# Optimization experiments

Measured on AMD Instinct MI355X. Metric: run time of the kernel, lower is better.

Reference implementation:

```python
import jax, jax.numpy as jnp
import numpy as np

B, D, H = 131072, 128, 64  # batch, input_dim (down_ch), output_dim


def _lstm(x, h, c, w_ih, w_hh, b):
    # torch nn.LSTMCell math; gate order i, f, g, o
    gates = x @ w_ih.T + h @ w_hh.T + b
    i, f, g, o = jnp.split(gates, 4, axis=-1)
    c2 = jax.nn.sigmoid(f) * c + jax.nn.sigmoid(i) * jnp.tanh(g)
    h2 = jax.nn.sigmoid(o) * jnp.tanh(c2)
    return h2, c2


def _lstm0(x, w_ih, b):
    # LSTMCell with zero initial (h, c): h-term and f*c term vanish
    gates = x @ w_ih.T + b
    i, f, g, o = jnp.split(gates, 4, axis=-1)
    c2 = jax.nn.sigmoid(i) * jnp.tanh(g)
    h2 = jax.nn.sigmoid(o) * jnp.tanh(c2)
    return h2, c2


def _trans(x, w, stride):
    # trans(): Conv1d(1,1,k=3,stride,pad=1,bias=False) + softmax(dim=-1)
    # x: [N, W], w: [1, 1, 3]
    y = jax.lax.conv_general_dilated(x[:, None, :], w, (stride,), [(1, 1)],
                                     dimension_numbers=('NCH', 'OIH', 'NCH'))
    return jax.nn.softmax(y[:, 0, :], axis=-1)


def _forward(spec, fw_ih1, fw_hh1, fb1, fw_ih2, fw_hh2, fb2, fw_ih3, fw_hh3, fb3,
             fw_ih4, fw_hh4, fb4, bw_ih1, bw_hh1, bb1, bw_ih2, bw_hh2, bb2,
             bw_ih3, bw_hh3, bb3, bw_ih4, bw_hh4, bb4,
             ft12h, ft12c, ft23h, ft23c, ft34h,
             bt43h, bt43c, bt32h, bt32c, bt21h, bt21c):
    b = spec.shape[0]
    # multi-scale chunking of spec: x2=[b,2,64], x3=[b,4,32], x4=[b,8,16]
    x2 = spec.reshape(b, 2, D // 2)
    x3 = spec.reshape(b, 4, D // 4)
    x4 = spec.reshape(b, 8, D // 8)

    # ---- fwd_LSTM (short memory): coarse -> fine, trans stride 2 ----
    # every cell call uses a state taken from the previous scale's backup, so
    # all steps at a scale are independent -> fully vectorized over steps.
    h1, c1 = _lstm0(spec, fw_ih1, fb1)                                      # [b,64]
    hb = _trans(h1, ft12h, 2)                                               # [b,32]
    cb = _trans(c1, ft12c, 2)
    h2, c2 = _lstm(x2, hb[:, None, :], cb[:, None, :], fw_ih2, fw_hh2, fb2)  # [b,2,32]
    hb2 = _trans(h2.reshape(b * 2, 32), ft23h, 2).reshape(b, 2, 16)
    cb2 = _trans(c2.reshape(b * 2, 32), ft23c, 2).reshape(b, 2, 16)
    h3, c3 = _lstm(x3, jnp.repeat(hb2, 2, axis=1), jnp.repeat(cb2, 2, axis=1),
                   fw_ih3, fw_hh3, fb3)                                     # [b,4,16]
    hb3 = _trans(h3.reshape(b * 4, 16), ft34h, 2).reshape(b, 4, 8)
    cb3 = _trans(c3.reshape(b * 4, 16), ft34h, 2).reshape(b, 4, 8)  # original bug: trans3_4h reused for cx
    h4, _ = _lstm(x4, jnp.repeat(hb3, 2, axis=1), jnp.repeat(cb3, 2, axis=1),
                  fw_ih4, fw_hh4, fb4)                                      # [b,8,8]
    out_fwd = h4.reshape(b, 64)

    # ---- bwd_LSTM (long memory): fine -> coarse, trans stride 1 over pairs ----
    h4b, c4b = _lstm0(x4, bw_ih4, bb4)                                      # [b,8,8] (zero state each step)
    # pairs of consecutive steps concatenated along features == reshape(b,4,16)
    hb4 = _trans(h4b.reshape(b * 4, 16), bt43h, 1).reshape(b, 4, 16)
    cb4 = _trans(c4b.reshape(b * 4, 16), bt43c, 1).reshape(b, 4, 16)
    h3b, c3b = _lstm(x3, hb4, cb4, bw_ih3, bw_hh3, bb3)                     # [b,4,16]
    hb3b = _trans(h3b.reshape(b * 2, 32), bt32h, 1).reshape(b, 2, 32)
    cb3b = _trans(c3b.reshape(b * 2, 32), bt32c, 1).reshape(b, 2, 32)
    h2b, c2b = _lstm(x2, hb3b, cb3b, bw_ih2, bw_hh2, bb2)                   # [b,2,32]
    hb1b = _trans(h2b.reshape(b, 64), bt21h, 1)                             # [b,64]
    cb1b = _trans(c2b.reshape(b, 64), bt21c, 1)
    _, c1b = _lstm(spec, hb1b, cb1b, bw_ih1, bw_hh1, bb1)                   # [b,64]

    return jnp.concatenate([out_fwd, c1b], axis=-1)                         # [b,128]


def setup_inputs() -> dict:
    key = jax.random.key(0)
    ks = iter(jax.random.split(key, 64))

    def nrm(shape, s=0.08):
        return (jax.random.normal(next(ks), shape) * s).astype(jnp.float32)

    inp = {"spec": jax.random.normal(next(ks), (B, D), dtype=jnp.float32)}
    dims = [(D, H), (D // 2, H // 2), (D // 4, H // 4), (D // 8, H // 8)]
    for pre in ("f", "b"):
        for idx, (di, dh) in enumerate(dims, 1):
            inp[f"{pre}w_ih{idx}"] = nrm((4 * dh, di))
            inp[f"{pre}w_hh{idx}"] = nrm((4 * dh, dh))
            inp[f"{pre}b{idx}"] = nrm((4 * dh,))
    for name in ("ft12h", "ft12c", "ft23h", "ft23c", "ft34h",
                 "bt43h", "bt43c", "bt32h", "bt32c", "bt21h", "bt21c"):
        inp[name] = nrm((1, 1, 3), 0.5)
    return inp


def reference(spec, fw_ih1, fw_hh1, fb1, fw_ih2, fw_hh2, fb2, fw_ih3, fw_hh3, fb3,
              fw_ih4, fw_hh4, fb4, bw_ih1, bw_hh1, bb1, bw_ih2, bw_hh2, bb2,
              bw_ih3, bw_hh3, bb3, bw_ih4, bw_hh4, bb4,
              ft12h, ft12c, ft23h, ft23c, ft34h,
              bt43h, bt43c, bt32h, bt32c, bt21h, bt21c):
    return _forward(spec, fw_ih1, fw_hh1, fb1, fw_ih2, fw_hh2, fb2, fw_ih3, fw_hh3,
                    fb3, fw_ih4, fw_hh4, fb4, bw_ih1, bw_hh1, bb1, bw_ih2, bw_hh2,
                    bb2, bw_ih3, bw_hh3, bb3, bw_ih4, bw_hh4, bb4,
                    ft12h, ft12c, ft23h, ft23c, ft34h,
                    bt43h, bt43c, bt32h, bt32c, bt21h, bt21c)
```

## Files before the change

### kernel.cpp

```cpp
#include <hip/hip_runtime.h>

typedef __attribute__((ext_vector_type(4))) float f32x4;
typedef __attribute__((ext_vector_type(8))) short short8;

#define DEV __device__ __forceinline__

DEV float fastrcp(float x){ return __builtin_amdgcn_rcpf(x); }
DEV float sigm(float x){ return fastrcp(1.f + __expf(-x)); }
DEV float tanh_(float x){ return 1.f - 2.f*fastrcp(__expf(2.f*x)+1.f); }
DEV unsigned short f2bf(float f){ unsigned u=__float_as_uint(f); u += 0x7fffu + ((u>>16)&1u); return (unsigned short)(u>>16); }
DEV float bf2f(unsigned short h){ return __uint_as_float(((unsigned)h)<<16); }
DEV unsigned pack2(float a, float b){ return (unsigned)f2bf(a) | ((unsigned)f2bf(b)<<16); }

DEV int gmask(int f){ return ((f&1)<<5) | (f&2) | ((f&4)<<2); }
DEV void stBF(char* A, int f, int b, float v){ *(unsigned short*)(A + (((f<<6) + (b ^ gmask(f)))<<1)) = f2bf(v); }
DEV float ldBF(const char* A, int f, int b){ return bf2f(*(const unsigned short*)(A + (((f<<6) + (b ^ gmask(f)))<<1))); }

DEV short8 frag(const char* p){ return *(const short8*)p; }
DEV short8 gfrag(const char* p){ return *(const short8*)p; }
DEV f32x4 MF(short8 a, short8 b, f32x4 c){ return __builtin_amdgcn_mfma_f32_16x16x32_bf16(a,b,c,0,0,0); }

struct P {
  const float *spec;
  const float *fw_ih1,*fw_hh1,*fb1,*fw_ih2,*fw_hh2,*fb2,*fw_ih3,*fw_hh3,*fb3,*fw_ih4,*fw_hh4,*fb4;
  const float *bw_ih1,*bw_hh1,*bb1,*bw_ih2,*bw_hh2,*bb2,*bw_ih3,*bw_hh3,*bb3,*bw_ih4,*bw_hh4,*bb4;
  const float *ft12h,*ft12c,*ft23h,*ft23c,*ft34h,*bt43h,*bt43c,*bt32h,*bt32c,*bt21h,*bt21c;
  float *out;
};

#define OF1 0
#define OF2 48
#define OF3 72
#define OF4 80
#define OB4 86
#define OB3 90
#define OB2 98
#define OB1 122
#define BLOBB (194*1024)

__global__ __launch_bounds__(256) void dsgsf_prep(P p, char* blob){
  int s = blockIdx.x;
  if (s == 3 || s == 4){
    bool isF = (s == 3);
    const float* wih = isF ? p.fw_ih4 : p.bw_ih4;
    const float* whh = p.fw_hh4;
    int nslot = isF ? 6 : 4;
    int off   = isF ? OF4 : OB4;
    for (int n = threadIdx.x; n < nslot*64; n += 256){
      int st = n>>6, lx = n&63;
      int R = lx&15, half = R>>3, feat = R&7;
      int k0 = ((lx>>4)<<3);
      unsigned dw[4];
      #pragma unroll
      for (int q=0;q<4;++q){
        float a=0.f, bv=0.f;
        int ka=k0+2*q, kb=ka+1;
        if (isF){
          if (st < 4){
            int pp = st>>1, t = st&1;
            int gi = t*2 + half;
            int src = gi*8 + feat, base = pp*16;
            if (ka>=base && ka<base+16) a  = wih[src*16 + (ka-base)];
            if (kb>=base && kb<base+16) bv = wih[src*16 + (kb-base)];
          } else {
            int t = st-4; int gi = t*2 + half; int src = gi*8 + feat;
            if (ka<8) a  = whh[src*8+ka];
            if (kb<8) bv = whh[src*8+kb];
          }
        } else {
          int pp = st>>1, t = st&1;
          int gi = (t==0) ? (half? 2:0) : (half? -1:3);
          if (gi >= 0){
            int src = gi*8 + feat, base = pp*16;
            if (ka>=base && ka<base+16) a  = wih[src*16 + (ka-base)];
            if (kb>=base && kb<base+16) bv = wih[src*16 + (kb-base)];
          }
        }
        dw[q] = pack2(a,bv);
      }
      *(uint4*)(blob + (size_t)(off+st)*1024 + lx*16) = make_uint4(dw[0],dw[1],dw[2],dw[3]);
    }
    return;
  }
  const float* wih=nullptr; const float* whh=nullptr;
  int H=0,NG=0,Kx=0,KXT=0,Kh=0,KT=0,NT=0,off=0,o0=0,o1=1,o2=2,o3=3;
  switch(s){
    case 0: wih=p.fw_ih1;               H=64;NG=3;Kx=128;KXT=4;Kh=0; KT=4;NT=12;off=OF1;o1=2;o2=3; break;
    case 1: wih=p.fw_ih2; whh=p.fw_hh2; H=32;NG=4;Kx=64; KXT=2;Kh=32;KT=3;NT=8; off=OF2; break;
    case 2: wih=p.fw_ih3; whh=p.fw_hh3; H=16;NG=4;Kx=32; KXT=1;Kh=16;KT=2;NT=4; off=OF3; break;
    case 5: wih=p.bw_ih3; whh=p.bw_hh3; H=16;NG=4;Kx=32; KXT=1;Kh=16;KT=2;NT=4; off=OB3; break;
    case 6: wih=p.bw_ih2; whh=p.bw_hh2; H=32;NG=4;Kx=64; KXT=2;Kh=32;KT=3;NT=8; off=OB2; break;
    default:wih=p.bw_ih1; whh=p.bw_hh1; H=64;NG=3;Kx=128;KXT=4;Kh=64;KT=6;NT=12;off=OB1; break;
  }
  int total = KT*NT*64;
  for (int n = threadIdx.x; n < total; n += 256){
    int kt = n/(NT*64); int rem = n - kt*NT*64; int nt = rem>>6; int lx = rem&63;
    int R = nt*16 + (lx&15);
    int gi = R / H; int feat = R - gi*H;
    int og = (gi==0)? o0 : (gi==1)? o1 : (gi==2)? o2 : o3;
    int src = og*H + feat;
    int k0 = kt*32 + ((lx>>4)<<3);
    unsigned dw[4];
    #pragma unroll
    for (int q=0;q<4;++q){
      float a=0.f, b=0.f;
      int ka=k0+2*q, kb=ka+1;
      if (gi < NG){
        if (ka < Kx) a = wih[(size_t)src*Kx + ka];
        else { int kh = ka - KXT*32; if (kh>=0 && kh<Kh) a = whh[(size_t)src*Kh + kh]; }
        if (kb < Kx) b = wih[(size_t)src*Kx + kb];
        else { int kh = kb - KXT*32; if (kh>=0 && kh<Kh) b = whh[(size_t)src*Kh + kh]; }
      }
      dw[q] = pack2(a,b);
    }
    *(uint4*)(blob + (size_t)off*1024 + (size_t)(kt*NT + nt)*1024 + lx*16) =
        make_uint4(dw[0],dw[1],dw[2],dw[3]);
  }
}

template<int NG,int NFT,int KT, class AF>
DEV void gemm_reg(f32x4 (&acc)[2][NG], const char* bstage, int nf, int mtp, int l, AF af){
  constexpr int NT = NG*NFT;
  #pragma unroll
  for (int kt=0; kt<KT; ++kt){
    short8 a0 = af(kt, mtp*2);
    short8 a1 = af(kt, mtp*2+1);
    #pragma unroll
    for (int g=0; g<NG; ++g){
      short8 bf = gfrag(bstage + (size_t)(kt*NT + g*NFT + nf)*1024 + l*16);
      acc[0][g] = MF(a0, bf, acc[0][g]);
      acc[1][g] = MF(a1, bf, acc[1][g]);
    }
  }
}

template<int NG>
DEV void binit(f32x4 (&acc)[2][NG], const float* bias, int H, int feat,
               int o0, int o1, int o2, int o3){
  int og[4] = {o0,o1,o2,o3};
  #pragma unroll
  for (int g=0; g<NG; ++g){
    float bv = bias[og[g]*H + feat];
    f32x4 v = {bv,bv,bv,bv};
    acc[0][g]=v; acc[1][g]=v;
  }
}

DEV void pw4(const f32x4 (&acc)[2][4], char* AH, char* AC, const char* BC,
             int arow, int cbrow, int mtp, int l){
  #pragma unroll
  for (int mtI=0;mtI<2;++mtI){
    #pragma unroll
    for (int r=0;r<4;++r){
      int batch = (mtp*2+mtI)*16 + ((l>>4)<<2) + r;
      float cb = ldBF(BC, cbrow, batch);
      float c = sigm(acc[mtI][1][r])*cb + sigm(acc[mtI][0][r])*tanh_(acc[mtI][2][r]);
      float h = sigm(acc[mtI][3][r])*tanh_(c);
      stBF(AH, arow, batch, h);
      stBF(AC, arow, batch, c);
    }
  }
}

template<int L,int S,int NO>
DEV void convE(const char* Ain, int row0, const float* tw, int o0, int b,
               float (&y)[NO], float& s){
  float w0=tw[0], w1=tw[1], w2=tw[2];
  s = 0.f;
  #pragma unroll
  for (int j=0;j<NO;++j){
    int o=o0+j, c=S*o;
    float v = w1*ldBF(Ain,row0+c,b);
    if (c>=1)   v += w0*ldBF(Ain,row0+c-1,b);
    if (c+1<L)  v += w2*ldBF(Ain,row0+c+1,b);
    y[j] = __expf(v); s += y[j];
  }
}
template<int SZ,int NO>
DEV void wrTF(char* TFb, int subBase, int o0, int b, const float (&y)[NO], float inv){
  #pragma unroll
  for (int g8=0; g8<NO/8; ++g8){
    int oo = o0 + g8*8, fl = oo&31;
    char* base = TFb + (size_t)((subBase+(oo>>5))*4+(b>>4))*SZ + ((b&15)+16*(fl>>3))*16;
    unsigned d0=pack2(y[g8*8+0]*inv,y[g8*8+1]*inv), d1=pack2(y[g8*8+2]*inv,y[g8*8+3]*inv);
    unsigned d2=pack2(y[g8*8+4]*inv,y[g8*8+5]*inv), d3=pack2(y[g8*8+6]*inv,y[g8*8+7]*inv);
    *(uint4*)base = make_uint4(d0,d1,d2,d3);
  }
}
template<int NO>
DEV void wrBC(char* BCb, int row0, int b, const float (&y)[NO], float inv){
  #pragma unroll
  for (int j=0;j<NO;++j) stBF(BCb, row0+j, b, y[j]*inv);
}

__global__ __launch_bounds__(512, 4) void dsgsf_main(P p, const char* blob){
  __shared__ __align__(16) char SM[51200];
  char* XP = SM;
  char* AH = SM + 16384;
  char* AC = SM + 24576;
  char* BC = SM + 32768;
  char* TF = SM + 40960;
  float* PSm = (float*)(SM + 49152);

  const int tid = threadIdx.x;
  const int l   = tid & 63;
  const int wu  = __builtin_amdgcn_readfirstlane(tid >> 6);
  const int mtp = wu & 1, z = wu >> 1;
  const long b0 = (long)blockIdx.x * 64;

  #pragma unroll
  for (int it=0; it<2; ++it){
    int n = it*512 + tid; int slot = n>>6, lx = n&63;
    int kc = slot>>2, mt = slot&3;
    const float* sp = p.spec + (b0 + mt*16 + (lx&15))*128 + kc*32 + ((lx>>4)<<3);
    float4 v0 = *(const float4*)sp; float4 v1 = *(const float4*)(sp+4);
    unsigned* dst = (unsigned*)(XP + (size_t)slot*1024 + lx*16);
    dst[0]=pack2(v0.x,v0.y); dst[1]=pack2(v0.z,v0.w);
    dst[2]=pack2(v1.x,v1.y); dst[3]=pack2(v1.z,v1.w);
  }
  __syncthreads();

  {
    f32x4 acc[2][3];
    int feat = z*16 + (l&15);
    binit<3>(acc, p.fb1, 64, feat, 0,2,3,0);
    auto af = [&](int kt, int mt){ return frag(XP + (size_t)((kt<<2)+mt)*1024 + l*16); };
    gemm_reg<3,4,4>(acc, blob + (size_t)OF1*1024, z, mtp, l, af);
    #pragma unroll
    for (int mtI=0;mtI<2;++mtI)
      #pragma unroll
      for (int r=0;r<4;++r){
        int batch = (mtp*2+mtI)*16 + ((l>>4)<<2) + r;
        float c = sigm(acc[mtI][0][r])*tanh_(acc[mtI][1][r]);
        float h = sigm(acc[mtI][2][r])*tanh_(c);
        stBF(AH, feat, batch, h); stBF(AC, feat, batch, c);
      }
  }
  __syncthreads();

  {
    float y[8], s;
    if (wu<4) convE<64,2,8>(AH, 0, p.ft12h, wu*8, l, y, s);
    else      convE<64,2,8>(AC, 0, p.ft12c, (wu-4)*8, l, y, s);
    PSm[wu*64+l] = s;
    __syncthreads();
    float tot = (wu<4) ? PSm[0*64+l]+PSm[1*64+l]+PSm[2*64+l]+PSm[3*64+l]
                       : PSm[4*64+l]+PSm[5*64+l]+PSm[6*64+l]+PSm[7*64+l];
    float inv = fastrcp(tot);
    if (wu<4) wrTF<1024,8>(TF, 0, wu*8, l, y, inv);
    else      wrBC<8>(BC, (wu-4)*8, l, y, inv);
  }
  __syncthreads();

  {
    f32x4 acc[2][4];
    int step = z>>1, nf = z&1;
    int feat = nf*16 + (l&15);
    binit<4>(acc, p.fb2, 32, feat, 0,1,2,3);
    auto af = [&](int kt, int mt){
      return (kt<2) ? frag(XP + (size_t)(((2*step+kt)<<2)+mt)*1024 + l*16)
                    : frag(TF + (size_t)mt*1024 + l*16); };
    gemm_reg<4,2,3>(acc, blob + (size_t)OF2*1024, nf, mtp, l, af);
    pw4(acc, AH, AC, BC, step*32+feat, feat, mtp, l);
  }
  __syncthreads();

  {
    float y[8], s; int v=wu&3, st=v>>1, ch=v&1;
    if (wu<4) convE<32,2,8>(AH, st*32, p.ft23h, ch*8, l, y, s);
    else      convE<32,2,8>(AC, st*32, p.ft23c, ch*8, l, y, s);
    PSm[wu*64+l] = s;
    __syncthreads();
    int base = (wu&4) | (st<<1);
    float inv = fastrcp(PSm[base*64+l] + PSm[(base|1)*64+l]);
    if (wu<4) wrTF<512,8>(TF, st, ch*8, l, y, inv);
    else      wrBC<8>(BC, st*16+ch*8, l, y, inv);
  }
  __syncthreads();

  {
    f32x4 acc[2][4];
    int s = z, feat = l&15;
    binit<4>(acc, p.fb3, 16, feat, 0,1,2,3);
    auto af = [&](int kt, int mt){
      return (kt==0) ? frag(XP + (size_t)((s<<2)+mt)*1024 + l*16)
                     : frag(TF + (size_t)(((s>>1)<<2)+mt)*512 + (l&31)*16); };
    gemm_reg<4,1,2>(acc, blob + (size_t)OF3*1024, 0, mtp, l, af);
    pw4(acc, AH, AC, BC, s*16+feat, (s>>1)*16+feat, mtp, l);
  }
  __syncthreads();

  {
    float y[8], s;
    if (wu<4){ convE<16,2,8>(AH, wu*16, p.ft34h, 0, l, y, s);
               wrTF<256,8>(TF, wu, 0, l, y, fastrcp(s)); }
    else     { convE<16,2,8>(AC, (wu-4)*16, p.ft34h, 0, l, y, s);
               wrBC<8>(BC, (wu-4)*8, l, y, fastrcp(s)); }
  }
  __syncthreads();

  {
    f32x4 a4[2][2][2];
    float bv0 = p.fb4[l&15], bv1 = p.fb4[16+(l&15)];
    #pragma unroll
    for (int uu=0;uu<2;++uu)
      #pragma unroll
      for (int mtI=0;mtI<2;++mtI){ a4[uu][mtI][0]=f32x4{bv0,bv0,bv0,bv0}; a4[uu][mtI][1]=f32x4{bv1,bv1,bv1,bv1}; }
    const char* bs = blob + (size_t)OF4*1024;
    short8 A0 = frag(XP + (size_t)((z<<2)+mtp*2  )*1024 + l*16);
    short8 A1 = frag(XP + (size_t)((z<<2)+mtp*2+1)*1024 + l*16);
    short8 H0 = frag(TF + (size_t)((z<<2)+mtp*2  )*256 + (l&15)*16);
    short8 H1 = frag(TF + (size_t)((z<<2)+mtp*2+1)*256 + (l&15)*16);
    short8 bh0 = gfrag(bs + 4*1024 + l*16);
    short8 bh1 = gfrag(bs + 5*1024 + l*16);
    #pragma unroll
    for (int uu=0;uu<2;++uu){
      short8 bx0 = gfrag(bs + (uu*2+0)*1024 + l*16);
      short8 bx1 = gfrag(bs + (uu*2+1)*1024 + l*16);
      a4[uu][0][0]=MF(A0,bx0,a4[uu][0][0]); a4[uu][0][1]=MF(A0,bx1,a4[uu][0][1]);
      a4[uu][1][0]=MF(A1,bx0,a4[uu][1][0]); a4[uu][1][1]=MF(A1,bx1,a4[uu][1][1]);
      a4[uu][0][0]=MF(H0,bh0,a4[uu][0][0]); a4[uu][0][1]=MF(H0,bh1,a4[uu][0][1]);
      a4[uu][1][0]=MF(H1,bh0,a4[uu][1][0]); a4[uu][1][1]=MF(H1,bh1,a4[uu][1][1]);
    }
    #pragma unroll
    for (int uu=0;uu<2;++uu)
      #pragma unroll
      for (int mtI=0;mtI<2;++mtI)
        #pragma unroll
        for (int r=0;r<4;++r){
          float iv = a4[uu][mtI][0][r], gv = a4[uu][mtI][1][r];
          float xf = __shfl_xor(iv,8), xo = __shfl_xor(gv,8);
          if ((l&15)<8){
            int q = l&15, u = z*2+uu;
            int batch = (mtp*2+mtI)*16 + ((l>>4)<<2) + r;
            float cb = ldBF(BC, (u>>1)*8+q, batch);
            float c = sigm(xf)*cb + sigm(iv)*tanh_(gv);
            float h = sigm(xo)*tanh_(c);
            p.out[(size_t)(b0+batch)*128 + u*8 + q] = h;
          }
        }
  }

  {
    f32x4 a4[2][2][2];
    float bv0 = ((l&15)<8) ? p.bb4[l&15] : p.bb4[(l&15)+8];
    float bv1 = ((l&15)<8) ? p.bb4[24+(l&15)] : 0.f;
    #pragma unroll
    for (int uu=0;uu<2;++uu)
      #pragma unroll
      for (int mtI=0;mtI<2;++mtI){ a4[uu][mtI][0]=f32x4{bv0,bv0,bv0,bv0}; a4[uu][mtI][1]=f32x4{bv1,bv1,bv1,bv1}; }
    const char* bs = blob + (size_t)OB4*1024;
    short8 A0 = frag(XP + (size_t)((z<<2)+mtp*2  )*1024 + l*16);
    short8 A1 = frag(XP + (size_t)((z<<2)+mtp*2+1)*1024 + l*16);
    #pragma unroll
    for (int uu=0;uu<2;++uu){
      short8 bx0 = gfrag(bs + (uu*2+0)*1024 + l*16);
      short8 bx1 = gfrag(bs + (uu*2+1)*1024 + l*16);
      a4[uu][0][0]=MF(A0,bx0,a4[uu][0][0]); a4[uu][0][1]=MF(A0,bx1,a4[uu][0][1]);
      a4[uu][1][0]=MF(A1,bx0,a4[uu][1][0]); a4[uu][1][1]=MF(A1,bx1,a4[uu][1][1]);
    }
    #pragma unroll
    for (int uu=0;uu<2;++uu)
      #pragma unroll
      for (int mtI=0;mtI<2;++mtI)
        #pragma unroll
        for (int r=0;r<4;++r){
          float iv = a4[uu][mtI][0][r], ov = a4[uu][mtI][1][r];
          float gv = __shfl_xor(iv,8);
          if ((l&15)<8){
            int q = l&15, u = z*2+uu;
            int batch = (mtp*2+mtI)*16 + ((l>>4)<<2) + r;
            float c = sigm(iv)*tanh_(gv);
            float h = sigm(ov)*tanh_(c);
            stBF(AH, u*8+q, batch, h); stBF(AC, u*8+q, batch, c);
          }
        }
  }
  __syncthreads();

  {
    float y[16], s;
    if (wu<4){ convE<16,1,16>(AH, wu*16, p.bt43h, 0, l, y, s);
               wrTF<512,16>(TF, wu, 0, l, y, fastrcp(s)); }
    else     { convE<16,1,16>(AC, (wu-4)*16, p.bt43c, 0, l, y, s);
               wrBC<16>(BC, (wu-4)*16, l, y, fastrcp(s)); }
  }
  __syncthreads();

  {
    f32x4 acc[2][4];
    int s = z, feat = l&15;
    binit<4>(acc, p.bb3, 16, feat, 0,1,2,3);
    auto af = [&](int kt, int mt){
      return (kt==0) ? frag(XP + (size_t)((s<<2)+mt)*1024 + l*16)
                     : frag(TF + (size_t)((s<<2)+mt)*512 + (l&31)*16); };
    gemm_reg<4,1,2>(acc, blob + (size_t)OB3*1024, 0, mtp, l, af);
    pw4(acc, AH, AC, BC, s*16+feat, s*16+feat, mtp, l);
  }
  __syncthreads();

  {
    float y[16], s; int v=wu&3, st=v>>1, ch=v&1;
    if (wu<4) convE<32,1,16>(AH, st*32, p.bt32h, ch*16, l, y, s);
    else      convE<32,1,16>(AC, st*32, p.bt32c, ch*16, l, y, s);
    PSm[wu*64+l] = s;
    __syncthreads();
    int base = (wu&4) | (st<<1);
    float inv = fastrcp(PSm[base*64+l] + PSm[(base|1)*64+l]);
    if (wu<4) wrTF<1024,16>(TF, st, ch*16, l, y, inv);
    else      wrBC<16>(BC, st*32+ch*16, l, y, inv);
  }
  __syncthreads();

  {
    f32x4 acc[2][4];
    int t2 = z>>1, nf = z&1;
    int feat = nf*16 + (l&15);
    binit<4>(acc, p.bb2, 32, feat, 0,1,2,3);
    auto af = [&](int kt, int mt){
      return (kt<2) ? frag(XP + (size_t)(((2*t2+kt)<<2)+mt)*1024 + l*16)
                    : frag(TF + (size_t)((t2<<2)+mt)*1024 + l*16); };
    gemm_reg<4,2,3>(acc, blob + (size_t)OB2*1024, nf, mtp, l, af);
    pw4(acc, AH, AC, BC, t2*32+feat, t2*32+feat, mtp, l);
  }
  __syncthreads();

  {
    float y[16], s;
    if (wu<4) convE<64,1,16>(AH, 0, p.bt21h, wu*16, l, y, s);
    else      convE<64,1,16>(AC, 0, p.bt21c, (wu-4)*16, l, y, s);
    PSm[wu*64+l] = s;
    __syncthreads();
    float tot = (wu<4) ? PSm[0*64+l]+PSm[1*64+l]+PSm[2*64+l]+PSm[3*64+l]
                       : PSm[4*64+l]+PSm[5*64+l]+PSm[6*64+l]+PSm[7*64+l];
    float inv = fastrcp(tot);
    if (wu<4) wrTF<1024,16>(TF, 0, wu*16, l, y, inv);
    else      wrBC<16>(BC, (wu-4)*16, l, y, inv);
  }
  __syncthreads();

  {
    f32x4 acc[2][3];
    int feat = z*16 + (l&15);
    binit<3>(acc, p.bb1, 64, feat, 0,1,2,0);
    auto af = [&](int kt, int mt){
      return (kt<4) ? frag(XP + (size_t)((kt<<2)+mt)*1024 + l*16)
                    : frag(TF + (size_t)(((kt-4)<<2)+mt)*1024 + l*16); };
    gemm_reg<3,4,6>(acc, blob + (size_t)OB1*1024, z, mtp, l, af);
    #pragma unroll
    for (int mtI=0;mtI<2;++mtI)
      #pragma unroll
      for (int r=0;r<4;++r){
        int batch = (mtp*2+mtI)*16 + ((l>>4)<<2) + r;
        float cb = ldBF(BC, feat, batch);
        float c = sigm(acc[mtI][1][r])*cb + sigm(acc[mtI][0][r])*tanh_(acc[mtI][2][r]);
        p.out[(size_t)(b0+batch)*128 + 64 + feat] = c;
      }
  }
}

extern "C" void kernel_launch(void* const* d_in, const int* in_sizes, int n_in,
                              void* d_out, int out_size, void* d_ws, size_t ws_size,
                              hipStream_t stream) {
  if (ws_size < (size_t)BLOBB) return;
  P p;
  p.spec   = (const float*)d_in[0];
  p.fw_ih1 = (const float*)d_in[1];  p.fw_hh1 = (const float*)d_in[2];  p.fb1 = (const float*)d_in[3];
  p.fw_ih2 = (const float*)d_in[4];  p.fw_hh2 = (const float*)d_in[5];  p.fb2 = (const float*)d_in[6];
  p.fw_ih3 = (const float*)d_in[7];  p.fw_hh3 = (const float*)d_in[8];  p.fb3 = (const float*)d_in[9];
  p.fw_ih4 = (const float*)d_in[10]; p.fw_hh4 = (const float*)d_in[11]; p.fb4 = (const float*)d_in[12];
  p.bw_ih1 = (const float*)d_in[13]; p.bw_hh1 = (const float*)d_in[14]; p.bb1 = (const float*)d_in[15];
  p.bw_ih2 = (const float*)d_in[16]; p.bw_hh2 = (const float*)d_in[17]; p.bb2 = (const float*)d_in[18];
  p.bw_ih3 = (const float*)d_in[19]; p.bw_hh3 = (const float*)d_in[20]; p.bb3 = (const float*)d_in[21];
  p.bw_ih4 = (const float*)d_in[22]; p.bw_hh4 = (const float*)d_in[23]; p.bb4 = (const float*)d_in[24];
  p.ft12h = (const float*)d_in[25]; p.ft12c = (const float*)d_in[26];
  p.ft23h = (const float*)d_in[27]; p.ft23c = (const float*)d_in[28];
  p.ft34h = (const float*)d_in[29];
  p.bt43h = (const float*)d_in[30]; p.bt43c = (const float*)d_in[31];
  p.bt32h = (const float*)d_in[32]; p.bt32c = (const float*)d_in[33];
  p.bt21h = (const float*)d_in[34]; p.bt21c = (const float*)d_in[35];
  p.out = (float*)d_out;

  char* blob = (char*)d_ws;
  hipLaunchKernelGGL(dsgsf_prep, dim3(8), dim3(256), 0, stream, p, blob);
  int Bn = in_sizes[0] / 128;
  hipLaunchKernelGGL(dsgsf_main, dim3(Bn/64), dim3(512), 0, stream, p, (const char*)blob);
}
```

Measured before the change: 179.1 us.

## Use hardware bf16 pack, exp2 intrinsics, paired LDS stores and sliding-window convs

Replaces the manual round-to-nearest bf16 conversion with the v_cvt_pk_bf16_f32 instruction and switches sigmoid/tanh/softmax exponentials to the raw exp2 intrinsic with folded log2e scaling. Pointwise LSTM epilogues now pack two batch elements per 32-bit LDS store instead of 16-bit stores. The conv+softmax helpers are split into stride-1 and stride-2 versions that reuse loaded neighbours in a sliding window, removing redundant LDS loads and boundary branches. Together these cut ALU and LDS instruction count in an elementwise-heavy fused kernel, at the cost of relying on paired stores landing contiguously under the swizzle and slightly different rounding of the exp path.

```diff
diff --git a/kernel.cpp b/kernel.cpp
--- a/kernel.cpp
+++ b/kernel.cpp
@@ -6,14 +6,20 @@
 #define DEV __device__ __forceinline__
 
 DEV float fastrcp(float x){ return __builtin_amdgcn_rcpf(x); }
-DEV float sigm(float x){ return fastrcp(1.f + __expf(-x)); }
-DEV float tanh_(float x){ return 1.f - 2.f*fastrcp(__expf(2.f*x)+1.f); }
-DEV unsigned short f2bf(float f){ unsigned u=__float_as_uint(f); u += 0x7fffu + ((u>>16)&1u); return (unsigned short)(u>>16); }
+DEV float exp2r(float x){ return __builtin_amdgcn_exp2f(x); }
+DEV float sigm(float x){ return fastrcp(1.f + exp2r(x*-1.44269504f)); }
+DEV float tanh_(float x){ return 1.f - 2.f*fastrcp(exp2r(x*2.88539008f)+1.f); }
+
+DEV unsigned cvtpk(float lo, float hi){ unsigned r; asm("v_cvt_pk_bf16_f32 %0, %1, %2" : "=v"(r) : "v"(lo), "v"(hi)); return r; }
+DEV unsigned short f2bf(float f){ return (unsigned short)cvtpk(f,f); }
 DEV float bf2f(unsigned short h){ return __uint_as_float(((unsigned)h)<<16); }
-DEV unsigned pack2(float a, float b){ return (unsigned)f2bf(a) | ((unsigned)f2bf(b)<<16); }
+DEV unsigned pack2(float a, float b){ return cvtpk(a,b); }
 
 DEV int gmask(int f){ return ((f&1)<<5) | (f&2) | ((f&4)<<2); }
 DEV void stBF(char* A, int f, int b, float v){ *(unsigned short*)(A + (((f<<6) + (b ^ gmask(f)))<<1)) = f2bf(v); }
+DEV void stBFpair(char* A, int f, int b, float v0, float v1){
+  *(unsigned*)(A + (((f<<6) + (b ^ gmask(f)))<<1)) = cvtpk(v0, v1);
+}
 DEV float ldBF(const char* A, int f, int b){ return bf2f(*(const unsigned short*)(A + (((f<<6) + (b ^ gmask(f)))<<1))); }
 
 DEV short8 frag(const char* p){ return *(const short8*)p; }
@@ -150,30 +156,53 @@
              int arow, int cbrow, int mtp, int l){
   #pragma unroll
   for (int mtI=0;mtI<2;++mtI){
+    float hv[4], cv[4];
+    int bb = (mtp*2+mtI)*16 + ((l>>4)<<2);
     #pragma unroll
     for (int r=0;r<4;++r){
-      int batch = (mtp*2+mtI)*16 + ((l>>4)<<2) + r;
-      float cb = ldBF(BC, cbrow, batch);
-      float c = sigm(acc[mtI][1][r])*cb + sigm(acc[mtI][0][r])*tanh_(acc[mtI][2][r]);
-      float h = sigm(acc[mtI][3][r])*tanh_(c);
-      stBF(AH, arow, batch, h);
-      stBF(AC, arow, batch, c);
-    }
-  }
-}
-
-template<int L,int S,int NO>
-DEV void convE(const char* Ain, int row0, const float* tw, int o0, int b,
-               float (&y)[NO], float& s){
-  float w0=tw[0], w1=tw[1], w2=tw[2];
+      float cb = ldBF(BC, cbrow, bb + r);
+      cv[r] = sigm(acc[mtI][1][r])*cb + sigm(acc[mtI][0][r])*tanh_(acc[mtI][2][r]);
+      hv[r] = sigm(acc[mtI][3][r])*tanh_(cv[r]);
+    }
+    stBFpair(AH, arow, bb,   hv[0], hv[1]);
+    stBFpair(AH, arow, bb+2, hv[2], hv[3]);
+    stBFpair(AC, arow, bb,   cv[0], cv[1]);
+    stBFpair(AC, arow, bb+2, cv[2], cv[3]);
+  }
+}
+
+template<int L,int NO>
+DEV void convE1(const char* Ain, int row0, const float* tw, int o0, int b,
+                float (&y)[NO], float& s){
+  float w0=tw[0]*1.44269504f, w1=tw[1]*1.44269504f, w2=tw[2]*1.44269504f;
   s = 0.f;
+  float prev = (o0 >= 1) ? ldBF(Ain, row0+o0-1, b) : 0.f;
+  float cur  = ldBF(Ain, row0+o0, b);
   #pragma unroll
   for (int j=0;j<NO;++j){
-    int o=o0+j, c=S*o;
-    float v = w1*ldBF(Ain,row0+c,b);
-    if (c>=1)   v += w0*ldBF(Ain,row0+c-1,b);
-    if (c+1<L)  v += w2*ldBF(Ain,row0+c+1,b);
-    y[j] = __expf(v); s += y[j];
+    int c = o0 + j;
+    float nxt;
+    if (j < NO-1) nxt = ldBF(Ain, row0+c+1, b);
+    else          nxt = (o0+NO < L) ? ldBF(Ain, row0+c+1, b) : 0.f;
+    float v = w0*prev + w1*cur + w2*nxt;
+    y[j] = exp2r(v); s += y[j];
+    prev = cur; cur = nxt;
+  }
+}
+template<int L,int NO>
+DEV void convE2(const char* Ain, int row0, const float* tw, int o0, int b,
+                float (&y)[NO], float& s){
+  float w0=tw[0]*1.44269504f, w1=tw[1]*1.44269504f, w2=tw[2]*1.44269504f;
+  s = 0.f;
+  float left = (o0 >= 1) ? ldBF(Ain, row0+2*o0-1, b) : 0.f;
+  #pragma unroll
+  for (int j=0;j<NO;++j){
+    int c = 2*(o0+j);
+    float mid = ldBF(Ain, row0+c,   b);
+    float rgt = ldBF(Ain, row0+c+1, b);
+    float v = w0*left + w1*mid + w2*rgt;
+    y[j] = exp2r(v); s += y[j];
+    left = rgt;
   }
 }
 template<int SZ,int NO>
@@ -182,8 +211,8 @@
   for (int g8=0; g8<NO/8; ++g8){
     int oo = o0 + g8*8, fl = oo&31;
     char* base = TFb + (size_t)((subBase+(oo>>5))*4+(b>>4))*SZ + ((b&15)+16*(fl>>3))*16;
-    unsigned d0=pack2(y[g8*8+0]*inv,y[g8*8+1]*inv), d1=pack2(y[g8*8+2]*inv,y[g8*8+3]*inv);
-    unsigned d2=pack2(y[g8*8+4]*inv,y[g8*8+5]*inv), d3=pack2(y[g8*8+6]*inv,y[g8*8+7]*inv);
+    unsigned d0=cvtpk(y[g8*8+0]*inv,y[g8*8+1]*inv), d1=cvtpk(y[g8*8+2]*inv,y[g8*8+3]*inv);
+    unsigned d2=cvtpk(y[g8*8+4]*inv,y[g8*8+5]*inv), d3=cvtpk(y[g8*8+6]*inv,y[g8*8+7]*inv);
     *(uint4*)base = make_uint4(d0,d1,d2,d3);
   }
 }
@@ -214,9 +243,9 @@
     int kc = slot>>2, mt = slot&3;
     const float* sp = p.spec + (b0 + mt*16 + (lx&15))*128 + kc*32 + ((lx>>4)<<3);
     float4 v0 = *(const float4*)sp; float4 v1 = *(const float4*)(sp+4);
-    unsigned* dst = (unsigned*)(XP + (size_t)slot*1024 + lx*16);
-    dst[0]=pack2(v0.x,v0.y); dst[1]=pack2(v0.z,v0.w);
-    dst[2]=pack2(v1.x,v1.y); dst[3]=pack2(v1.z,v1.w);
+    unsigned d0=cvtpk(v0.x,v0.y), d1=cvtpk(v0.z,v0.w);
+    unsigned d2=cvtpk(v1.x,v1.y), d3=cvtpk(v1.z,v1.w);
+    *(uint4*)(XP + (size_t)slot*1024 + lx*16) = make_uint4(d0,d1,d2,d3);
   }
   __syncthreads();
 
@@ -227,21 +256,26 @@
     auto af = [&](int kt, int mt){ return frag(XP + (size_t)((kt<<2)+mt)*1024 + l*16); };
     gemm_reg<3,4,4>(acc, blob + (size_t)OF1*1024, z, mtp, l, af);
     #pragma unroll
-    for (int mtI=0;mtI<2;++mtI)
+    for (int mtI=0;mtI<2;++mtI){
+      float hv[4], cv[4];
+      int bb = (mtp*2+mtI)*16 + ((l>>4)<<2);
       #pragma unroll
       for (int r=0;r<4;++r){
-        int batch = (mtp*2+mtI)*16 + ((l>>4)<<2) + r;
-        float c = sigm(acc[mtI][0][r])*tanh_(acc[mtI][1][r]);
-        float h = sigm(acc[mtI][2][r])*tanh_(c);
-        stBF(AH, feat, batch, h); stBF(AC, feat, batch, c);
+        cv[r] = sigm(acc[mtI][0][r])*tanh_(acc[mtI][1][r]);
+        hv[r] = sigm(acc[mtI][2][r])*tanh_(cv[r]);
       }
+      stBFpair(AH, feat, bb,   hv[0], hv[1]);
+      stBFpair(AH, feat, bb+2, hv[2], hv[3]);
+      stBFpair(AC, feat, bb,   cv[0], cv[1]);
+      stBFpair(AC, feat, bb+2, cv[2], cv[3]);
+    }
   }
   __syncthreads();
 
   {
     float y[8], s;
-    if (wu<4) convE<64,2,8>(AH, 0, p.ft12h, wu*8, l, y, s);
-    else      convE<64,2,8>(AC, 0, p.ft12c, (wu-4)*8, l, y, s);
+    if (wu<4) convE2<64,8>(AH, 0, p.ft12h, wu*8, l, y, s);
+    else      convE2<64,8>(AC, 0, p.ft12c, (wu-4)*8, l, y, s);
     PSm[wu*64+l] = s;
     __syncthreads();
     float tot = (wu<4) ? PSm[0*64+l]+PSm[1*64+l]+PSm[2*64+l]+PSm[3*64+l]
@@ -267,8 +301,8 @@
 
   {
     float y[8], s; int v=wu&3, st=v>>1, ch=v&1;
-    if (wu<4) convE<32,2,8>(AH, st*32, p.ft23h, ch*8, l, y, s);
-    else      convE<32,2,8>(AC, st*32, p.ft23c, ch*8, l, y, s);
+    if (wu<4) convE2<32,8>(AH, st*32, p.ft23h, ch*8, l, y, s);
+    else      convE2<32,8>(AC, st*32, p.ft23c, ch*8, l, y, s);
     PSm[wu*64+l] = s;
     __syncthreads();
     int base = (wu&4) | (st<<1);
@@ -292,9 +326,9 @@
 
   {
     float y[8], s;
-    if (wu<4){ convE<16,2,8>(AH, wu*16, p.ft34h, 0, l, y, s);
+    if (wu<4){ convE2<16,8>(AH, wu*16, p.ft34h, 0, l, y, s);
                wrTF<256,8>(TF, wu, 0, l, y, fastrcp(s)); }
-    else     { convE<16,2,8>(AC, (wu-4)*16, p.ft34h, 0, l, y, s);
+    else     { convE2<16,8>(AC, (wu-4)*16, p.ft34h, 0, l, y, s);
                wrBC<8>(BC, (wu-4)*8, l, y, fastrcp(s)); }
   }
   __syncthreads();
@@ -362,27 +396,32 @@
     #pragma unroll
     for (int uu=0;uu<2;++uu)
       #pragma unroll
-      for (int mtI=0;mtI<2;++mtI)
+      for (int mtI=0;mtI<2;++mtI){
+        float hv[4], cv[4];
         #pragma unroll
         for (int r=0;r<4;++r){
           float iv = a4[uu][mtI][0][r], ov = a4[uu][mtI][1][r];
           float gv = __shfl_xor(iv,8);
-          if ((l&15)<8){
-            int q = l&15, u = z*2+uu;
-            int batch = (mtp*2+mtI)*16 + ((l>>4)<<2) + r;
-            float c = sigm(iv)*tanh_(gv);
-            float h = sigm(ov)*tanh_(c);
-            stBF(AH, u*8+q, batch, h); stBF(AC, u*8+q, batch, c);
-          }
+          cv[r] = sigm(iv)*tanh_(gv);
+          hv[r] = sigm(ov)*tanh_(cv[r]);
         }
+        if ((l&15)<8){
+          int q = l&15, u = z*2+uu, f = u*8+q;
+          int bb = (mtp*2+mtI)*16 + ((l>>4)<<2);
+          stBFpair(AH, f, bb,   hv[0], hv[1]);
+          stBFpair(AH, f, bb+2, hv[2], hv[3]);
+          stBFpair(AC, f, bb,   cv[0], cv[1]);
+          stBFpair(AC, f, bb+2, cv[2], cv[3]);
+        }
+      }
   }
   __syncthreads();
 
   {
     float y[16], s;
-    if (wu<4){ convE<16,1,16>(AH, wu*16, p.bt43h, 0, l, y, s);
+    if (wu<4){ convE1<16,16>(AH, wu*16, p.bt43h, 0, l, y, s);
                wrTF<512,16>(TF, wu, 0, l, y, fastrcp(s)); }
-    else     { convE<16,1,16>(AC, (wu-4)*16, p.bt43c, 0, l, y, s);
+    else     { convE1<16,16>(AC, (wu-4)*16, p.bt43c, 0, l, y, s);
                wrBC<16>(BC, (wu-4)*16, l, y, fastrcp(s)); }
   }
   __syncthreads();
@@ -401,8 +440,8 @@
 
   {
     float y[16], s; int v=wu&3, st=v>>1, ch=v&1;
-    if (wu<4) convE<32,1,16>(AH, st*32, p.bt32h, ch*16, l, y, s);
-    else      convE<32,1,16>(AC, st*32, p.bt32c, ch*16, l, y, s);
+    if (wu<4) convE1<32,16>(AH, st*32, p.bt32h, ch*16, l, y, s);
+    else      convE1<32,16>(AC, st*32, p.bt32c, ch*16, l, y, s);
     PSm[wu*64+l] = s;
     __syncthreads();
     int base = (wu&4) | (st<<1);
@@ -427,8 +466,8 @@
 
   {
     float y[16], s;
-    if (wu<4) convE<64,1,16>(AH, 0, p.bt21h, wu*16, l, y, s);
-    else      convE<64,1,16>(AC, 0, p.bt21c, (wu-4)*16, l, y, s);
+    if (wu<4) convE1<64,16>(AH, 0, p.bt21h, wu*16, l, y, s);
+    else      convE1<64,16>(AC, 0, p.bt21c, (wu-4)*16, l, y, s);
     PSm[wu*64+l] = s;
     __syncthreads();
     float tot = (wu<4) ? PSm[0*64+l]+PSm[1*64+l]+PSm[2*64+l]+PSm[3*64+l]
```

After: 162.9 us. 1.1x faster.
